# Kernel tuning notes

Hardware: AMD Instinct MI355X
Metric: run time of the kernel (lower is better)

## Reference

```python
import jax, jax.numpy as jnp
import numpy as np
from jax import lax


def conv2d(x, w, b, stride=1, pad=1):
    y = lax.conv_general_dilated(x, w, (stride, stride), [(pad, pad), (pad, pad)],
                                 dimension_numbers=('NCHW', 'OIHW', 'NCHW'))
    return y + b[None, :, None, None]


def nearest_resize(x, H, W):
    # torch F.interpolate(mode='nearest'): src = floor(dst * in / out)
    h, w = x.shape[-2:]
    iy = (jnp.arange(H) * h) // H
    ix = (jnp.arange(W) * w) // W
    return x[:, :, iy[:, None], ix[None, :]]


def deform_conv2d(x, offset, w, b):
    # torchvision DeformConv2d: kernel 3x3, stride 1, pad 1, dilation 1, 1 offset group
    B, C, H, W = x.shape
    K = 9
    off = offset.reshape(B, K, 2, H, W)  # per kernel tap: (dy, dx)
    dy = (jnp.arange(K) // 3 - 1).astype(x.dtype)
    dx = (jnp.arange(K) % 3 - 1).astype(x.dtype)
    yy = jnp.arange(H, dtype=x.dtype)[None, None, :, None]
    xx = jnp.arange(W, dtype=x.dtype)[None, None, None, :]
    py = yy + dy[None, :, None, None] + off[:, :, 0]  # [B,K,H,W] sample rows
    px = xx + dx[None, :, None, None] + off[:, :, 1]  # [B,K,H,W] sample cols
    y0 = jnp.floor(py)
    x0 = jnp.floor(px)
    ly = py - y0
    lx = px - x0
    y0i = y0.astype(jnp.int32)
    x0i = x0.astype(jnp.int32)
    x_flat = x.reshape(B, C, H * W)

    def gather(yi, xi, wgt):
        # zero contribution for out-of-bounds corners (torchvision zero padding)
        valid = (yi >= 0) & (yi < H) & (xi >= 0) & (xi < W)
        idx = (jnp.clip(yi, 0, H - 1) * W + jnp.clip(xi, 0, W - 1)).reshape(B, -1)
        vals = jax.vmap(lambda xf, i: xf[:, i])(x_flat, idx)  # [B, C, K*H*W]
        wv = (wgt * valid.astype(x.dtype)).reshape(B, 1, -1)
        return vals * wv

    s = gather(y0i, x0i, (1 - ly) * (1 - lx))
    s = s + gather(y0i, x0i + 1, (1 - ly) * lx)
    s = s + gather(y0i + 1, x0i, ly * (1 - lx))
    s = s + gather(y0i + 1, x0i + 1, ly * lx)
    s = s.reshape(B, C, K, H * W)  # bilinear-sampled taps
    O = w.shape[0]
    out = jnp.einsum('bckn,ock->bon', s, w.reshape(O, C, K))
    return out.reshape(B, O, H, W) + b[None, :, None, None]


def setup_inputs() -> dict:
    key = jax.random.key(0)
    ks = jax.random.split(key, 12)
    B, Ccnn, H, W = 8, 768, 28, 28
    Cvit, hv, wv = 3840, 14, 14
    d_hidn, Cout = 512, 768

    def he(k, shape):
        fan_in = shape[1] * shape[2] * shape[3]
        return jax.random.normal(k, shape, jnp.float32) * np.float32(np.sqrt(2.0 / fan_in))

    return {
        'cnn_feat': jax.random.normal(ks[0], (B, Ccnn, H, W), jnp.float32),
        'vit_feat': jax.random.normal(ks[1], (B, Cvit, hv, wv), jnp.float32),
        'w_off': he(ks[2], (18, Cvit, 3, 3)),
        'b_off': jnp.zeros((18,), jnp.float32),
        'w_def': he(ks[3], (Cout, Ccnn, 3, 3)),
        'b_def': jax.random.normal(ks[4], (Cout,), jnp.float32) * 0.01,
        'w1': he(ks[5], (d_hidn, Cout, 3, 3)),
        'b1': jax.random.normal(ks[6], (d_hidn,), jnp.float32) * 0.01,
        'w2': he(ks[7], (Cout, d_hidn, 3, 3)),
        'b2': jax.random.normal(ks[8], (Cout,), jnp.float32) * 0.01,
    }


def reference(cnn_feat, vit_feat, w_off, b_off, w_def, b_def, w1, b1, w2, b2):
    H, W = cnn_feat.shape[-2:]
    v = nearest_resize(vit_feat, H, W)
    offset = conv2d(v, w_off, b_off)                 # [B,18,H,W]
    d = deform_conv2d(cnn_feat, offset, w_def, b_def)  # [B,768,H,W]
    h = jax.nn.relu(conv2d(d, w1, b1, stride=2))     # [B,512,H/2,W/2]
    return conv2d(h, w2, b2, stride=1)               # [B,768,H/2,W/2]
```

## Files before the change

kernel.cpp:

```cpp
#include <hip/hip_runtime.h>
#include <hip/hip_bf16.h>
#include <stdint.h>

typedef __attribute__((ext_vector_type(8))) short v8s;
typedef __attribute__((ext_vector_type(4))) short v4s;
typedef __attribute__((ext_vector_type(4))) float v4f;

__device__ __forceinline__ short f2bf(float f) {
  union { float f; uint32_t u; } v; v.f = f;
  uint32_t u = v.u;
  uint32_t r = (u + 0x7fffu + ((u >> 16) & 1u)) >> 16;
  return (short)r;
}
__device__ __forceinline__ float bf2f(short s) {
  union { uint32_t u; float f; } v;
  v.u = ((uint32_t)(uint16_t)s) << 16;
  return v.f;
}
__device__ __forceinline__ void gload16(const void* g, void* l) {
  __builtin_amdgcn_global_load_lds(
      (const __attribute__((address_space(1))) void*)g,
      (__attribute__((address_space(3))) void*)l, 16, 0, 0);
}

template<int OP, int OV, int C>
__global__ __launch_bounds__(256) void prep_w_panel(const float* __restrict__ w,
                                                    short* __restrict__ out) {
  int i = blockIdx.x * 256 + threadIdx.x;
  if (i >= OP * C * 9) return;
  int e = i & 7;
  int o = (i >> 3) % OP;
  int p = i / (8 * OP);
  int k = p * 8 + e;
  int tap = k / C, c = k % C;
  out[i] = (o < OV) ? f2bf(w[((size_t)o * C + c) * 9 + tap]) : (short)0;
}

__global__ __launch_bounds__(256) void prep_woff2_k(const float* __restrict__ w,
                                                    short* __restrict__ out) {
  int i = blockIdx.x * 256 + threadIdx.x;
  if (i >= 480 * 192 * 8) return;
  int e = i & 7;
  int m = (i >> 3) % 192;
  int kp = i / 1536;
  int c = kp * 8 + e;
  int o = m / 9, tap = m % 9;
  out[i] = (m < 162) ? f2bf(w[((size_t)o * 3840 + c) * 9 + tap]) : (short)0;
}

template<int C, int P>
__global__ __launch_bounds__(256) void transpose_k(const float* __restrict__ in,
                                                   short* __restrict__ out) {
  __shared__ float lds[32][65];
  int n0 = blockIdx.x * 64, c0 = blockIdx.y * 32;
  int t = threadIdx.x;
#pragma unroll
  for (int e = 0; e < 8; e++) {
    int id = e * 256 + t;
    int cl = id >> 6, nl = id & 63;
    int n = n0 + nl;
    if (n < 8 * P) {
      int b = n / P, p = n % P;
      lds[cl][nl] = in[((size_t)b * C + c0 + cl) * P + p];
    }
  }
  __syncthreads();
  int nl = t >> 2, cs = (t & 3) * 8;
  int n = n0 + nl;
  if (n < 8 * P) {
    v8s v;
#pragma unroll
    for (int i = 0; i < 8; i++) v[i] = f2bf(lds[cs + i][nl]);
    *(v8s*)(out + (size_t)n * C + c0 + cs) = v;
  }
}

template<int MODE, int BM, int BN, int WGM, int AO, int CIN, int KSPLIT,
         int NVALID, int IH, int IW, int OW, int STRIDE, int PART>
__global__ __launch_bounds__(256) void gemm_k(const short* __restrict__ Ap,
                                              const short* __restrict__ Bp,
                                              const float* __restrict__ bias,
                                              void* __restrict__ dst,
                                              const short* __restrict__ zp) {
  constexpr int WGN = 4 / WGM;
  constexpr int WM = BM / WGM, WN = BN / WGN;
  constexpr int MF = WM / 16, NF = WN / 16;
  constexpr int CHA = BM * 8, CHT = (BM + BN) * 8;
  constexpr int NT = KSPLIT / 64;

  __shared__ __align__(16) short SM[2][CHT * 8];

  const int tid = threadIdx.x;
  const int lane = tid & 63, wid = tid >> 6;
  const int wm = wid / WGN, wn = wid % WGN;
  int bx = blockIdx.x, by = blockIdx.y;
  if constexpr (MODE == 1) {
    int bid = by * 98 + bx;
    int xcd = bid & 7, idx = bid >> 3;
    constexpr int q = 73, r = 4;
    int wg = (xcd < r ? xcd * (q + 1) : r * (q + 1) + (xcd - r) * q) + idx;
    by = wg % 6; bx = wg / 6;
  }
  const int n0 = bx * BN, m0 = by * BM;
  const int ts = blockIdx.z;
  const int kbeg = ts * KSPLIT;
  const int lrow = lane & 15, lkg = lane >> 4;

  v4f acc[MF][NF];
#pragma unroll
  for (int i = 0; i < MF; i++)
#pragma unroll
    for (int j = 0; j < NF; j++) acc[i][j] = (v4f){0.f, 0.f, 0.f, 0.f};

  auto stage = [&](int k, int buf) {
#pragma unroll
    for (int it = 0; it < CHT / 256; it++) {
      int ch = it * 256 + tid;
      const short* src;
      if (ch < CHA) {
        int kg = ch / BM, row = ch % BM;
        src = Ap + ((size_t)((k >> 3) + kg) * AO + m0 + row) * 8;
      } else {
        int bch = ch - CHA;
        int kg = bch / BN, col = bch % BN;
        int gk = k + kg * 8;
        int n = n0 + col;
        if constexpr (MODE == 0) {
          src = (n < NVALID) ? Bp + ((size_t)n * 3840 + gk) : zp;
        } else if constexpr (MODE == 1) {
          src = Bp + ((size_t)(gk >> 3) * 6272 + n) * 8;
        } else {
          int tap = gk / CIN, cc = gk % CIN;
          int b = n / (OW * OW), rem = n % (OW * OW);
          int oy = rem / OW, ox = rem % OW;
          int py = oy * STRIDE + tap / 3 - 1, px = ox * STRIDE + tap % 3 - 1;
          src = (n < NVALID && py >= 0 && py < IH && px >= 0 && px < IW)
                  ? Bp + ((size_t)((b * IH + py) * IW + px) * CIN + cc)
                  : zp;
        }
      }
      gload16(src, &SM[buf][(size_t)(it * 256 + (tid & ~63)) * 8]);
    }
  };

  stage(kbeg, 0);
  __syncthreads();
  int buf = 0;
  for (int t = 0; t < NT; ++t) {
    if (t + 1 < NT) stage(kbeg + (t + 1) * 64, buf ^ 1);
    v8s af[2][MF], bfv[2][NF];
#pragma unroll
    for (int s = 0; s < 2; s++) {
#pragma unroll
      for (int mf = 0; mf < MF; mf++)
        af[s][mf] = *(const v8s*)(&SM[buf][(size_t)((s * 4 + lkg) * BM + wm * WM + mf * 16 + lrow) * 8]);
#pragma unroll
      for (int nf = 0; nf < NF; nf++)
        bfv[s][nf] = *(const v8s*)(&SM[buf][(size_t)(CHA + (s * 4 + lkg) * BN + wn * WN + nf * 16 + lrow) * 8]);
    }
#pragma unroll
    for (int s = 0; s < 2; s++)
#pragma unroll
      for (int mf = 0; mf < MF; mf++)
#pragma unroll
        for (int nf = 0; nf < NF; nf++)
          acc[mf][nf] = __builtin_amdgcn_mfma_f32_16x16x32_bf16(af[s][mf], bfv[s][nf], acc[mf][nf], 0, 0, 0);
    __syncthreads();
    buf ^= 1;
  }

#pragma unroll
  for (int mf = 0; mf < MF; mf++) {
    int gm = m0 + wm * WM + mf * 16 + lkg * 4;
#pragma unroll
    for (int nf = 0; nf < NF; nf++) {
      int gn = n0 + wn * WN + nf * 16 + lrow;
      v4f a4 = acc[mf][nf];
      if constexpr (MODE == 0) {
        float* part = (float*)dst;
        if (gn < NVALID) {
#pragma unroll
          for (int r = 0; r < 4; r++)
            part[((size_t)ts * AO + gm + r) * 1568 + gn] = a4[r];
        }
      } else if constexpr (MODE == 1) {
        short* dt = (short*)dst;
        v4s v;
#pragma unroll
        for (int r = 0; r < 4; r++) v[r] = f2bf(a4[r] + bias[gm + r]);
        *(v4s*)(dt + (size_t)gn * 768 + gm) = v;
      } else if constexpr (MODE == 2) {
        if (gn < NVALID) {
          if constexpr (PART) {
            float* pd = (float*)dst;
            *(v4f*)(pd + ((size_t)ts * 1568 + gn) * 512 + gm) = a4;
          } else {
            short* ht = (short*)dst;
            v4s v;
#pragma unroll
            for (int r = 0; r < 4; r++) v[r] = f2bf(fmaxf(a4[r] + bias[gm + r], 0.f));
            *(v4s*)(ht + (size_t)gn * 512 + gm) = v;
          }
        }
      } else {
        if (gn < NVALID) {
          if constexpr (PART) {
            float* pd = (float*)dst;
#pragma unroll
            for (int r = 0; r < 4; r++)
              pd[((size_t)(ts * 768) + gm + r) * 1568 + gn] = a4[r];
          } else {
            float* o = (float*)dst;
            int b = gn / 196, p = gn % 196;
#pragma unroll
            for (int r = 0; r < 4; r++)
              o[((size_t)(b * 768 + gm + r)) * 196 + p] = a4[r] + bias[gm + r];
          }
        }
      }
    }
  }
}

__global__ __launch_bounds__(256) void reduce_off2_k(const float* __restrict__ part,
                                                     const float* __restrict__ boff,
                                                     float* __restrict__ offs) {
  int i = blockIdx.x * 256 + threadIdx.x;
  if (i >= 8 * 18 * 784) return;
  int b = i / (18 * 784), r = i % (18 * 784);
  int o = r / 784, yx = r % 784;
  int y = yx / 28, x = yx % 28;
  float s = boff[o];
#pragma unroll
  for (int tap = 0; tap < 9; tap++) {
    int py = y + tap / 3 - 1, px = x + tap % 3 - 1;
    if (py >= 0 && py < 28 && px >= 0 && px < 28) {
      int n = b * 196 + (py >> 1) * 14 + (px >> 1);
      int m = o * 9 + tap;
#pragma unroll
      for (int z = 0; z < 4; z++)
        s += part[((size_t)z * 192 + m) * 1568 + n];
    }
  }
  offs[i] = s;
}

__global__ __launch_bounds__(256) void reduce_c1_k(const float* __restrict__ part,
                                                   const float* __restrict__ b1,
                                                   short* __restrict__ h_t) {
  int i = blockIdx.x * 256 + threadIdx.x;
  if (i >= 1568 * 128) return;
  int n = i >> 7, o4 = (i & 127) * 4;
  v4f s0 = *(const v4f*)(part + ((size_t)n) * 512 + o4);
  v4f s1 = *(const v4f*)(part + ((size_t)(1568 + n)) * 512 + o4);
  v4f bb = *(const v4f*)(b1 + o4);
  v4s v;
#pragma unroll
  for (int r = 0; r < 4; r++) v[r] = f2bf(fmaxf(s0[r] + s1[r] + bb[r], 0.f));
  *(v4s*)(h_t + (size_t)n * 512 + o4) = v;
}

__global__ __launch_bounds__(256) void reduce_c2_k(const float* __restrict__ part,
                                                   const float* __restrict__ b2,
                                                   float* __restrict__ out) {
  int i = blockIdx.x * 256 + threadIdx.x;
  if (i >= 768 * 392) return;
  int m = i / 392, n4 = (i % 392) * 4;
  v4f s0 = *(const v4f*)(part + (size_t)m * 1568 + n4);
  v4f s1 = *(const v4f*)(part + (size_t)(768 + m) * 1568 + n4);
  float bv = b2[m];
  int b = n4 / 196, p = n4 % 196;
  v4f o;
#pragma unroll
  for (int r = 0; r < 4; r++) o[r] = s0[r] + s1[r] + bv;
  *(v4f*)(out + ((size_t)(b * 768 + m)) * 196 + p) = o;
}

__global__ __launch_bounds__(256) void sample_k(const short* __restrict__ cnn_t,
                                                const float* __restrict__ offs,
                                                short* __restrict__ sp) {
  int n = blockIdx.x * 256 + threadIdx.x;
  if (n >= 6272) return;
  int tap = blockIdx.y;
  int ch0 = blockIdx.z * 48;
  int b = n / 784, yx = n % 784;
  int y = yx / 28, x = yx % 28;
  float dy = offs[((size_t)b * 18 + tap * 2 + 0) * 784 + yx];
  float dx = offs[((size_t)b * 18 + tap * 2 + 1) * 784 + yx];
  float py = (float)(y + tap / 3 - 1) + dy;
  float px = (float)(x + tap % 3 - 1) + dx;
  float fy = floorf(py), fx = floorf(px);
  float ly = py - fy, lx = px - fx;
  int y0 = (int)fy, x0 = (int)fx;
  int y1 = y0 + 1, x1 = x0 + 1;
  float vy0 = (y0 >= 0 && y0 < 28) ? 1.f : 0.f;
  float vy1 = (y1 >= 0 && y1 < 28) ? 1.f : 0.f;
  float vx0 = (x0 >= 0 && x0 < 28) ? 1.f : 0.f;
  float vx1 = (x1 >= 0 && x1 < 28) ? 1.f : 0.f;
  float w00 = (1.f - ly) * (1.f - lx) * vy0 * vx0;
  float w01 = (1.f - ly) * lx * vy0 * vx1;
  float w10 = ly * (1.f - lx) * vy1 * vx0;
  float w11 = ly * lx * vy1 * vx1;
  int cy0 = min(max(y0, 0), 27), cy1 = min(max(y1, 0), 27);
  int cx0 = min(max(x0, 0), 27), cx1 = min(max(x1, 0), 27);
  const short* base = cnn_t + (size_t)b * 784 * 768 + ch0 * 8;
  const short* p00 = base + (size_t)(cy0 * 28 + cx0) * 768;
  const short* p01 = base + (size_t)(cy0 * 28 + cx1) * 768;
  const short* p10 = base + (size_t)(cy1 * 28 + cx0) * 768;
  const short* p11 = base + (size_t)(cy1 * 28 + cx1) * 768;
  short* op = sp + ((size_t)(tap * 96 + ch0) * 6272 + n) * 8;
#pragma unroll 4
  for (int i = 0; i < 48; ++i) {
    v8s a = *(const v8s*)(p00 + i * 8);
    v8s bb = *(const v8s*)(p01 + i * 8);
    v8s c = *(const v8s*)(p10 + i * 8);
    v8s d = *(const v8s*)(p11 + i * 8);
    v8s o;
#pragma unroll
    for (int j = 0; j < 8; j++) {
      float v = w00 * bf2f(a[j]) + w01 * bf2f(bb[j]) + w10 * bf2f(c[j]) + w11 * bf2f(d[j]);
      o[j] = f2bf(v);
    }
    *(v8s*)op = o;
    op += (size_t)6272 * 8;
  }
}

extern "C" void kernel_launch(void* const* d_in, const int* in_sizes, int n_in,
                              void* d_out, int out_size, void* d_ws, size_t ws_size,
                              hipStream_t stream) {
  const float* cnn   = (const float*)d_in[0];
  const float* vit   = (const float*)d_in[1];
  const float* w_off = (const float*)d_in[2];
  const float* b_off = (const float*)d_in[3];
  const float* w_def = (const float*)d_in[4];
  const float* b_def = (const float*)d_in[5];
  const float* w1    = (const float*)d_in[6];
  const float* b1    = (const float*)d_in[7];
  const float* w2    = (const float*)d_in[8];
  const float* b2    = (const float*)d_in[9];
  float* out = (float*)d_out;
  char* ws = (char*)d_ws;

  short* wdef_p  = (short*)(ws + 0);
  short* w1_p    = (short*)(ws + 10616832);
  short* w2_p    = (short*)(ws + 17694720);
  short* woff2_p = (short*)(ws + 24772608);
  short* v_t     = (short*)(ws + 26247168);
  float* offs    = (float*)(ws + 38289408);
  float* part    = (float*)(ws + 38740992);
  short* sp      = (short*)(ws + 38740992);
  float* part1   = (float*)(ws + 38740992);
  float* part2   = (float*)(ws + 45163520);
  short* d_t     = (short*)(ws + 125445120);
  short* h_t     = (short*)(ws + 135078912);
  short* cnn_t   = (short*)(ws + 136684544);
  short* zp      = (short*)(ws + 146318336);

  hipMemsetAsync((void*)zp, 0, 256, stream);

  dim3 blk(256);
  prep_w_panel<768, 768, 768><<<(768 * 6912 + 255) / 256, blk, 0, stream>>>(w_def, wdef_p);
  prep_w_panel<512, 512, 768><<<(512 * 6912 + 255) / 256, blk, 0, stream>>>(w1, w1_p);
  prep_w_panel<768, 768, 512><<<(768 * 4608 + 255) / 256, blk, 0, stream>>>(w2, w2_p);
  prep_woff2_k<<<(480 * 192 * 8 + 255) / 256, blk, 0, stream>>>(w_off, woff2_p);
  transpose_k<3840, 196><<<dim3(25, 120), blk, 0, stream>>>(vit, v_t);
  transpose_k<768, 784><<<dim3(98, 24), blk, 0, stream>>>(cnn, cnn_t);

  gemm_k<0, 64, 64, 2, 192, 3840, 960, 1568, 14, 14, 14, 1, 0>
      <<<dim3(25, 3, 4), blk, 0, stream>>>(woff2_p, v_t, nullptr, part, zp);
  reduce_off2_k<<<441, blk, 0, stream>>>(part, b_off, offs);

  sample_k<<<dim3(25, 9, 2), blk, 0, stream>>>(cnn_t, offs, sp);

  gemm_k<1, 128, 64, 2, 768, 768, 6912, 6272, 28, 28, 28, 1, 0>
      <<<dim3(98, 6, 1), blk, 0, stream>>>(wdef_p, sp, b_def, d_t, zp);

  gemm_k<2, 64, 64, 2, 512, 768, 3456, 1568, 28, 28, 14, 2, 1>
      <<<dim3(25, 8, 2), blk, 0, stream>>>(w1_p, d_t, b1, part1, zp);
  reduce_c1_k<<<784, blk, 0, stream>>>(part1, b1, h_t);

  gemm_k<3, 64, 64, 2, 768, 512, 2304, 1568, 14, 14, 14, 1, 1>
      <<<dim3(25, 12, 2), blk, 0, stream>>>(w2_p, h_t, b2, part2, zp);
  reduce_c2_k<<<1176, blk, 0, stream>>>(part2, b2, out);
}
```

Measured before the change: 300.6 us.

## Fuse weight prep kernels, shrink deform GEMM tile, split sampling finer

```diff
diff --git a/kernel.cpp b/kernel.cpp
--- a/kernel.cpp
+++ b/kernel.cpp
@@ -23,29 +23,36 @@
       (__attribute__((address_space(3))) void*)l, 16, 0, 0);
 }
 
-template<int OP, int OV, int C>
-__global__ __launch_bounds__(256) void prep_w_panel(const float* __restrict__ w,
-                                                    short* __restrict__ out) {
+__global__ __launch_bounds__(256) void prep_all_k(const float* __restrict__ wdef,
+                                                  const float* __restrict__ w1,
+                                                  const float* __restrict__ w2,
+                                                  const float* __restrict__ woff,
+                                                  short* __restrict__ wdef_p,
+                                                  short* __restrict__ w1_p,
+                                                  short* __restrict__ w2_p,
+                                                  short* __restrict__ woff2_p) {
   int i = blockIdx.x * 256 + threadIdx.x;
-  if (i >= OP * C * 9) return;
-  int e = i & 7;
-  int o = (i >> 3) % OP;
-  int p = i / (8 * OP);
-  int k = p * 8 + e;
-  int tap = k / C, c = k % C;
-  out[i] = (o < OV) ? f2bf(w[((size_t)o * C + c) * 9 + tap]) : (short)0;
-}
-
-__global__ __launch_bounds__(256) void prep_woff2_k(const float* __restrict__ w,
-                                                    short* __restrict__ out) {
-  int i = blockIdx.x * 256 + threadIdx.x;
-  if (i >= 480 * 192 * 8) return;
-  int e = i & 7;
-  int m = (i >> 3) % 192;
-  int kp = i / 1536;
-  int c = kp * 8 + e;
-  int o = m / 9, tap = m % 9;
-  out[i] = (m < 162) ? f2bf(w[((size_t)o * 3840 + c) * 9 + tap]) : (short)0;
+  constexpr int R0 = 768 * 768 * 9;
+  constexpr int R1 = 512 * 768 * 9;
+  constexpr int R2 = 768 * 512 * 9;
+  constexpr int R3 = 480 * 192 * 8;
+  if (i < R0) {
+    int e = i & 7, o = (i >> 3) % 768, p = i / (8 * 768);
+    int k = p * 8 + e, tap = k / 768, c = k % 768;
+    wdef_p[i] = f2bf(wdef[((size_t)o * 768 + c) * 9 + tap]);
+  } else if ((i -= R0) < R1) {
+    int e = i & 7, o = (i >> 3) % 512, p = i / (8 * 512);
+    int k = p * 8 + e, tap = k / 768, c = k % 768;
+    w1_p[i] = f2bf(w1[((size_t)o * 768 + c) * 9 + tap]);
+  } else if ((i -= R1) < R2) {
+    int e = i & 7, o = (i >> 3) % 768, p = i / (8 * 768);
+    int k = p * 8 + e, tap = k / 512, c = k % 512;
+    w2_p[i] = f2bf(w2[((size_t)o * 512 + c) * 9 + tap]);
+  } else if ((i -= R2) < R3) {
+    int e = i & 7, m = (i >> 3) % 192, kp = i / 1536;
+    int c = kp * 8 + e, o = m / 9, tap = m % 9;
+    woff2_p[i] = (m < 162) ? f2bf(woff[((size_t)o * 3840 + c) * 9 + tap]) : (short)0;
+  }
 }
 
 template<int C, int P>
@@ -96,10 +103,8 @@
   int bx = blockIdx.x, by = blockIdx.y;
   if constexpr (MODE == 1) {
     int bid = by * 98 + bx;
-    int xcd = bid & 7, idx = bid >> 3;
-    constexpr int q = 73, r = 4;
-    int wg = (xcd < r ? xcd * (q + 1) : r * (q + 1) + (xcd - r) * q) + idx;
-    by = wg % 6; bx = wg / 6;
+    int wg = (bid & 7) * 147 + (bid >> 3);
+    by = wg % 12; bx = wg / 12;
   }
   const int n0 = bx * BN, m0 = by * BM;
   const int ts = blockIdx.z;
@@ -282,7 +287,7 @@
   int n = blockIdx.x * 256 + threadIdx.x;
   if (n >= 6272) return;
   int tap = blockIdx.y;
-  int ch0 = blockIdx.z * 48;
+  int ch0 = blockIdx.z * 24;
   int b = n / 784, yx = n % 784;
   int y = yx / 28, x = yx % 28;
   float dy = offs[((size_t)b * 18 + tap * 2 + 0) * 784 + yx];
@@ -310,7 +315,7 @@
   const short* p11 = base + (size_t)(cy1 * 28 + cx1) * 768;
   short* op = sp + ((size_t)(tap * 96 + ch0) * 6272 + n) * 8;
 #pragma unroll 4
-  for (int i = 0; i < 48; ++i) {
+  for (int i = 0; i < 24; ++i) {
     v8s a = *(const v8s*)(p00 + i * 8);
     v8s bb = *(const v8s*)(p01 + i * 8);
     v8s c = *(const v8s*)(p10 + i * 8);
@@ -360,10 +365,8 @@
   hipMemsetAsync((void*)zp, 0, 256, stream);
 
   dim3 blk(256);
-  prep_w_panel<768, 768, 768><<<(768 * 6912 + 255) / 256, blk, 0, stream>>>(w_def, wdef_p);
-  prep_w_panel<512, 512, 768><<<(512 * 6912 + 255) / 256, blk, 0, stream>>>(w1, w1_p);
-  prep_w_panel<768, 768, 512><<<(768 * 4608 + 255) / 256, blk, 0, stream>>>(w2, w2_p);
-  prep_woff2_k<<<(480 * 192 * 8 + 255) / 256, blk, 0, stream>>>(w_off, woff2_p);
+  prep_all_k<<<(13123584 + 255) / 256, blk, 0, stream>>>(
+      w_def, w1, w2, w_off, wdef_p, w1_p, w2_p, woff2_p);
   transpose_k<3840, 196><<<dim3(25, 120), blk, 0, stream>>>(vit, v_t);
   transpose_k<768, 784><<<dim3(98, 24), blk, 0, stream>>>(cnn, cnn_t);
 
@@ -371,10 +374,10 @@
       <<<dim3(25, 3, 4), blk, 0, stream>>>(woff2_p, v_t, nullptr, part, zp);
   reduce_off2_k<<<441, blk, 0, stream>>>(part, b_off, offs);
 
-  sample_k<<<dim3(25, 9, 2), blk, 0, stream>>>(cnn_t, offs, sp);
-
-  gemm_k<1, 128, 64, 2, 768, 768, 6912, 6272, 28, 28, 28, 1, 0>
-      <<<dim3(98, 6, 1), blk, 0, stream>>>(wdef_p, sp, b_def, d_t, zp);
+  sample_k<<<dim3(25, 9, 4), blk, 0, stream>>>(cnn_t, offs, sp);
+
+  gemm_k<1, 64, 64, 2, 768, 768, 6912, 6272, 28, 28, 28, 1, 0>
+      <<<dim3(98, 12, 1), blk, 0, stream>>>(wdef_p, sp, b_def, d_t, zp);
 
   gemm_k<2, 64, 64, 2, 512, 768, 3456, 1568, 28, 28, 14, 2, 1>
       <<<dim3(25, 8, 2), blk, 0, stream>>>(w1_p, d_t, b1, part1, zp);
```

New measurement: 352.3 us. +17.2%, slower.
